# Performance work log

Measured on AMD Instinct MI355X. Metric: run time of the kernel, lower is better.

## Reference

```python
import jax, jax.numpy as jnp
import numpy as np

B, L, D, C, N, K = 4096, 4096, 1024, 64, 8192, 5
TEMP = 0.1
ALPHA = 2.0
EPS = 1e-12


def setup_inputs() -> dict:
    key = jax.random.key(0)
    ks = jax.random.split(key, 8)
    x = jax.random.normal(ks[0], (B, 1, L), jnp.float32)
    y = jax.random.randint(ks[1], (B,), 0, C)
    Wf = jax.random.normal(ks[2], (L, D), jnp.float32) * 0.02
    Wc = jax.random.normal(ks[3], (C, D), jnp.float32) * 0.02
    bc = jnp.zeros((C,), jnp.float32)
    supports_old = jax.random.normal(ks[4], (N, D), jnp.float32)
    scores_old = jax.nn.softmax(jax.random.normal(ks[5], (N, C), jnp.float32), axis=-1)
    labels_old = jax.nn.one_hot(jax.random.randint(ks[6], (N,), 0, C), C, dtype=jnp.float32)
    return dict(x=x, y=y, Wf=Wf, Wc=Wc, bc=bc, supports_old=supports_old,
                labels_old=labels_old, scores_old=scores_old)


def _l2n(v, axis):
    return v / jnp.maximum(jnp.linalg.norm(v, axis=axis, keepdims=True), EPS)


def _masked_mean(v, w):
    return jnp.sum(v * w) / jnp.maximum(jnp.sum(w), 1.0)


def _tta_loss(x, Wf, Wc, bc, supports_old, labels_old, scores_old):
    feats = x.reshape(B, L) @ Wf                      # [B, D] featurizer
    logits = feats @ Wc.T + bc                        # [B, C]
    probs = jax.nn.softmax(logits, -1)
    logp = jax.nn.log_softmax(logits, -1)
    prob = probs.max(-1)
    pred = jnp.argmax(logits, -1)
    # prediction-confidence filter
    y_certain = prob >= prob.mean()
    # input-energy entropy filter (scipy.stats.entropy over axis=2)
    px = x * x
    px = px / jnp.maximum(px.sum(2, keepdims=True), EPS)
    e = -(px * jnp.log(px + 1e-30)).sum(2).reshape(B)
    e_certain = e < e.mean()
    w_c = (e_certain & y_certain).astype(jnp.float32)  # certain mask as weights
    w_u = 1.0 - w_c
    yhat = jax.nn.one_hot(pred, C, dtype=jnp.float32)
    # --- memory bank concat + prototype build (no_grad in torch) ---
    sup_all = jnp.concatenate([supports_old, feats], 0)        # [N+B, D]
    lab_all = jnp.concatenate([labels_old, yhat], 0)           # [N+B, C]
    w_all = jnp.concatenate([jnp.ones((N,), jnp.float32), w_c], 0)
    lw = lab_all * w_all[:, None]
    protos = _l2n(sup_all, 1).T @ lw / jnp.maximum(lw.sum(0, keepdims=True), EPS)
    protos = jax.lax.stop_gradient(_l2n(protos, 0))            # [D, C]
    # --- loss1: Tsallis entropy - diversity on balanced probs ---
    m = jnp.sum(probs * w_c[:, None], 0) / jnp.maximum(w_c.sum(), 1.0)
    pb = probs / jnp.maximum(m, EPS)
    pb = pb / pb.sum(1, keepdims=True)
    tsallis = jnp.mean((1.0 - jnp.sum(pb ** ALPHA, 1)) / (ALPHA - 1.0))
    pm = pb.mean(0)
    div = -jnp.sum(pm * jnp.log(pm + EPS))
    loss1 = tsallis - div
    # --- loss2: PCL, prototype CE on certain samples (temp=1) ---
    lp = jax.nn.log_softmax(_l2n(feats, 1) @ protos, -1)       # [B, C]
    ce = -jnp.take_along_axis(lp, pred[:, None], 1)[:, 0]
    loss2 = _masked_mean(ce, w_c)
    # --- loss3: NCL, kNN soft targets from memory bank, uncertain rows ---
    scores_all = jax.lax.stop_gradient(jnp.concatenate([scores_old, probs], 0))
    sup_det = jax.lax.stop_gradient(sup_all)
    sim = _l2n(feats, 1) @ _l2n(sup_det, 1).T / TEMP           # [B, N+B]
    sim = jnp.where(w_all[None, :] > 0, sim, -jnp.inf)
    _, idx = jax.lax.top_k(sim, K)                             # [B, K]
    tgt = scores_all[idx].mean(1)                              # [B, C]
    ncl = -(tgt * logp).sum(1)
    loss3 = _masked_mean(ncl, w_u)
    return loss1 + loss2 + loss3


def reference(x, y, Wf, Wc, bc, supports_old, labels_old, scores_old):
    return _tta_loss(x, Wf, Wc, bc, supports_old, labels_old, scores_old)
```

## Files before the change

kernel.cpp:

```cpp
#include <hip/hip_runtime.h>
#include <math.h>

#define BBATCH 4096
#define LLEN   4096
#define DDIM   1024
#define CCLS   64
#define NSUP   8192
#define NTOT   12288
#define FEPS   1e-12f
#define KCHUNK 48
#define KCAND  (KCHUNK*6)

#define SC_SUMP  0
#define SC_SUME  1
#define SC_SUMWC 2
#define SC_TSAL  3
#define SC_L2NUM 4
#define SC_L3NUM 5

typedef _Float16 half4_t __attribute__((ext_vector_type(4)));
typedef _Float16 half8_t __attribute__((ext_vector_type(8)));
typedef float    f32x4   __attribute__((ext_vector_type(4)));
typedef float    f32x16  __attribute__((ext_vector_type(16)));

static const size_t OFF_FEATS  = 0;
static const size_t OFF_FEATP1 = OFF_FEATS  + (size_t)BBATCH*DDIM;
static const size_t OFF_WFTH   = OFF_FEATP1 + (size_t)BBATCH*DDIM;
static const size_t OFF_WFTL   = OFF_WFTH   + (size_t)DDIM*LLEN/2;
static const size_t OFF_PROBS  = OFF_WFTL   + (size_t)DDIM*LLEN/2;
static const size_t OFF_LOGP   = OFF_PROBS  + (size_t)BBATCH*CCLS;
static const size_t OFF_FNORM  = OFF_LOGP   + (size_t)BBATCH*CCLS;
static const size_t OFF_SNORM  = OFF_FNORM  + BBATCH;
static const size_t OFF_PMAX   = OFF_SNORM  + NSUP;
static const size_t OFF_EROW   = OFF_PMAX   + BBATCH;
static const size_t OFF_WC     = OFF_EROW   + BBATCH;
static const size_t OFF_PRED   = OFF_WC     + BBATCH;
static const size_t OFF_RB     = OFF_PRED   + BBATCH;
static const size_t OFF_SNM    = OFF_RB     + BBATCH;
static const size_t OFF_PROTOT = OFF_SNM    + NTOT;
static const size_t OFF_CVAL   = OFF_PROTOT + (size_t)CCLS*DDIM;
static const size_t OFF_CIDX   = OFF_CVAL   + (size_t)BBATCH*KCAND;
static const size_t OFF_ZERO   = OFF_CIDX   + (size_t)BBATCH*KCAND;
static const size_t OFF_MACC   = OFF_ZERO;
static const size_t OFF_PMACC  = OFF_MACC   + CCLS;
static const size_t OFF_COLS   = OFF_PMACC  + CCLS;
static const size_t OFF_SCAL   = OFF_COLS   + CCLS;
static const size_t OFF_PROTUN = OFF_SCAL   + 32;
static const size_t OFF_ZEND   = OFF_PROTUN + (size_t)DDIM*CCLS;
static const size_t OFF_SUPH   = OFF_ZEND;
static const size_t OFF_SUPL   = OFF_SUPH   + (size_t)NSUP*DDIM/2;
static const size_t WS_END     = OFF_SUPL   + (size_t)NSUP*DDIM/2;

__device__ __forceinline__ float waveSum(float v){
  #pragma unroll
  for (int o = 32; o > 0; o >>= 1) v += __shfl_xor(v, o);
  return v;
}
__device__ __forceinline__ float waveMax(float v){
  #pragma unroll
  for (int o = 32; o > 0; o >>= 1) v = fmaxf(v, __shfl_xor(v, o));
  return v;
}
__device__ __forceinline__ float blockSum256(float v, float* sh4){
  v = waveSum(v);
  if ((threadIdx.x & 63) == 0) sh4[threadIdx.x >> 6] = v;
  __syncthreads();
  float r = sh4[0] + sh4[1] + sh4[2] + sh4[3];
  __syncthreads();
  return r;
}
__device__ __forceinline__ void top6_insert(float* v, int* ix, float s, int si){
  bool c0=s>v[0],c1=s>v[1],c2=s>v[2],c3=s>v[3],c4=s>v[4],c5=s>v[5];
  v[5]=c5?(c4?v[4]:s):v[5]; ix[5]=c5?(c4?ix[4]:si):ix[5];
  v[4]=c4?(c3?v[3]:s):v[4]; ix[4]=c4?(c3?ix[3]:si):ix[4];
  v[3]=c3?(c2?v[2]:s):v[3]; ix[3]=c3?(c2?ix[2]:si):ix[3];
  v[2]=c2?(c1?v[1]:s):v[2]; ix[2]=c2?(c1?ix[1]:si):ix[2];
  v[1]=c1?(c0?v[0]:s):v[1]; ix[1]=c1?(c0?ix[0]:si):ix[1];
  v[0]=c0?s:v[0];           ix[0]=c0?si:ix[0];
}
__device__ __forceinline__ void split4(const float4 v, half4_t* h, half4_t* l){
  half4_t hh, ll;
  hh[0] = (_Float16)v.x; hh[1] = (_Float16)v.y; hh[2] = (_Float16)v.z; hh[3] = (_Float16)v.w;
  ll[0] = (_Float16)(v.x - (float)hh[0]);
  ll[1] = (_Float16)(v.y - (float)hh[1]);
  ll[2] = (_Float16)(v.z - (float)hh[2]);
  ll[3] = (_Float16)(v.w - (float)hh[3]);
  *h = hh; *l = ll;
}
__device__ __forceinline__ void split8(const float4 a, const float4 b,
                                       half8_t* h, half8_t* l){
  half8_t hh, ll;
  hh[0]=(_Float16)a.x; hh[1]=(_Float16)a.y; hh[2]=(_Float16)a.z; hh[3]=(_Float16)a.w;
  hh[4]=(_Float16)b.x; hh[5]=(_Float16)b.y; hh[6]=(_Float16)b.z; hh[7]=(_Float16)b.w;
  ll[0]=(_Float16)(a.x-(float)hh[0]); ll[1]=(_Float16)(a.y-(float)hh[1]);
  ll[2]=(_Float16)(a.z-(float)hh[2]); ll[3]=(_Float16)(a.w-(float)hh[3]);
  ll[4]=(_Float16)(b.x-(float)hh[4]); ll[5]=(_Float16)(b.y-(float)hh[5]);
  ll[6]=(_Float16)(b.z-(float)hh[6]); ll[7]=(_Float16)(b.w-(float)hh[7]);
  *h = hh; *l = ll;
}

__global__ __launch_bounds__(256)
void k_entropy(const float* __restrict__ x, float* __restrict__ e_row,
               float* __restrict__ scal){
  __shared__ __align__(16) float lx[LLEN];
  __shared__ float sh4[4];
  int row = blockIdx.x, t = threadIdx.x;
  const float4* xr = (const float4*)(x + (size_t)row * LLEN);
  float s = 0.f;
  #pragma unroll
  for (int i = 0; i < 4; ++i){
    float4 v = xr[t + 256*i];
    ((float4*)lx)[t + 256*i] = v;
    s += v.x*v.x + v.y*v.y + v.z*v.z + v.w*v.w;
  }
  s = blockSum256(s, sh4);
  float inv = 1.0f / fmaxf(s, FEPS);
  float ent = 0.f;
  #pragma unroll
  for (int i = 0; i < 4; ++i){
    float4 v = ((float4*)lx)[t + 256*i];
    float p;
    p = v.x*v.x*inv; ent -= p * logf(p + 1e-30f);
    p = v.y*v.y*inv; ent -= p * logf(p + 1e-30f);
    p = v.z*v.z*inv; ent -= p * logf(p + 1e-30f);
    p = v.w*v.w*inv; ent -= p * logf(p + 1e-30f);
  }
  ent = blockSum256(ent, sh4);
  if (t == 0){ e_row[row] = ent; atomicAdd(&scal[SC_SUME], ent); }
}

__global__ __launch_bounds__(256)
void k_wft(const float* __restrict__ Wf, unsigned short* __restrict__ WftH,
           unsigned short* __restrict__ WftL){
  __shared__ __align__(16) float ld[64*68];
  int t = threadIdx.x;
  int d0 = blockIdx.x * 64;
  int l0 = blockIdx.y * 64;
  #pragma unroll
  for (int i = 0; i < 4; ++i){
    int flat = t + 256*i;
    int l = flat >> 4, d4 = (flat & 15) * 4;
    *(float4*)&ld[l*68 + d4] = *(const float4*)(Wf + (size_t)(l0+l)*DDIM + d0 + d4);
  }
  __syncthreads();
  #pragma unroll
  for (int i = 0; i < 4; ++i){
    int flat = t + 256*i;
    int d = flat >> 4, l4 = (flat & 15) * 4;
    float4 v = make_float4(ld[(l4+0)*68 + d], ld[(l4+1)*68 + d],
                           ld[(l4+2)*68 + d], ld[(l4+3)*68 + d]);
    half4_t h, l;
    split4(v, &h, &l);
    *(half4_t*)(WftH + (size_t)(d0+d)*LLEN + l0 + l4) = h;
    *(half4_t*)(WftL + (size_t)(d0+d)*LLEN + l0 + l4) = l;
  }
}

#define SUBH 4096

__global__ __launch_bounds__(256)
void k_feats_mfma(const float* __restrict__ X, const unsigned short* __restrict__ WftHu,
                  const unsigned short* __restrict__ WftLu, float* __restrict__ featp){
  __shared__ __align__(16) _Float16 lds[2*4*SUBH];
  int t = threadIdx.x;
  int n0 = blockIdx.x * 128;
  int m0 = blockIdx.y * 128;
  int kz = blockIdx.z;
  int w = t >> 6, lane = t & 63;
  int wr = w >> 1, wc = w & 1;
  int l31 = lane & 31, hi = lane >> 5;
  const _Float16* Bgh = (const _Float16*)WftHu + (size_t)n0*LLEN;
  const _Float16* Bgl = (const _Float16*)WftLu + (size_t)n0*LLEN;
  const size_t glRow = (size_t)(lane >> 2)*LLEN;
  int ra = t >> 1;
  int kg8 = (t & 1) * 16;
  int aswz = (ra >> 3) & 3;
  const float* Ag = X + (size_t)(m0 + ra)*LLEN + kg8;
  f32x16 acc[2][2];
  #pragma unroll
  for (int i=0;i<2;++i){
    #pragma unroll
    for (int j=0;j<2;++j) acc[i][j] = (f32x16)(0.f);
  }
  const int kstart = kz*2048;

  #define STAGE_B(bufi, k0c) do {                                                 \
    _Float16* Lb = lds + (bufi)*(4*SUBH);                                         \
    _Pragma("unroll")                                                             \
    for (int s2 = 0; s2 < 2; ++s2){                                               \
      int blk = s2*4 + w;                                                         \
      int csrc = (lane & 3) ^ ((blk*2 + (lane >> 5)) & 3);                        \
      size_t go = glRow + (size_t)blk*16*LLEN + (k0c) + (size_t)csrc*8;           \
      __builtin_amdgcn_global_load_lds(                                           \
        (const __attribute__((address_space(1))) void*)(Bgh + go),                \
        (__attribute__((address_space(3))) void*)(Lb + 2*SUBH + blk*512), 16,0,0);\
      __builtin_amdgcn_global_load_lds(                                           \
        (const __attribute__((address_space(1))) void*)(Bgl + go),                \
        (__attribute__((address_space(3))) void*)(Lb + 3*SUBH + blk*512), 16,0,0);\
    }                                                                             \
  } while(0)

  STAGE_B(0, kstart);
  float4 avs[4];
  #pragma unroll
  for (int i=0;i<4;++i) avs[i] = *(const float4*)(Ag + kstart + 4*i);
  int cur = 0;
  int swz = (l31 >> 3) & 3;
  for (int it = 0; it < 64; ++it){
    _Float16* Ah = lds + cur*(4*SUBH);
    _Float16* Al = Ah + SUBH;
    #pragma unroll
    for (int c2 = 0; c2 < 2; ++c2){
      half8_t hv, lv;
      split8(avs[2*c2], avs[2*c2+1], &hv, &lv);
      int slot = ((kg8 >> 3) + c2) ^ aswz;
      *(half8_t*)&Ah[ra*32 + slot*8] = hv;
      *(half8_t*)&Al[ra*32 + slot*8] = lv;
    }
    __syncthreads();
    if (it < 63){
      int kn = kstart + (it+1)*32;
      STAGE_B(cur ^ 1, kn);
      #pragma unroll
      for (int i=0;i<4;++i) avs[i] = *(const float4*)(Ag + kn + 4*i);
      __builtin_amdgcn_sched_barrier(0);
    }
    const _Float16* Bh = lds + cur*(4*SUBH) + 2*SUBH;
    const _Float16* Bl = Bh + SUBH;
    #pragma unroll
    for (int kf = 0; kf < 2; ++kf){
      int sc = (kf*2 + hi) ^ swz;
      half8_t ahf[2], alf[2], bhf[2], blf[2];
      #pragma unroll
      for (int mi=0;mi<2;++mi){
        int off = (wr*64 + mi*32 + l31)*32 + sc*8;
        ahf[mi] = *(const half8_t*)&Ah[off];
        alf[mi] = *(const half8_t*)&Al[off];
      }
      #pragma unroll
      for (int ni=0;ni<2;++ni){
        int off = (wc*64 + ni*32 + l31)*32 + sc*8;
        bhf[ni] = *(const half8_t*)&Bh[off];
        blf[ni] = *(const half8_t*)&Bl[off];
      }
      #pragma unroll
      for (int mi=0;mi<2;++mi){
        #pragma unroll
        for (int ni=0;ni<2;++ni){
          acc[mi][ni] = __builtin_amdgcn_mfma_f32_32x32x16_f16(ahf[mi], bhf[ni], acc[mi][ni], 0,0,0);
          acc[mi][ni] = __builtin_amdgcn_mfma_f32_32x32x16_f16(ahf[mi], blf[ni], acc[mi][ni], 0,0,0);
          acc[mi][ni] = __builtin_amdgcn_mfma_f32_32x32x16_f16(alf[mi], bhf[ni], acc[mi][ni], 0,0,0);
        }
      }
    }
    cur ^= 1;
  }
  #undef STAGE_B
  float* outp = featp + (size_t)kz * BBATCH * DDIM;
  #pragma unroll
  for (int mi=0;mi<2;++mi){
    #pragma unroll
    for (int ni=0;ni<2;++ni){
      #pragma unroll
      for (int r=0;r<16;++r){
        int row = m0 + wr*64 + mi*32 + (r&3) + 8*(r>>2) + 4*hi;
        int col = n0 + wc*64 + ni*32 + l31;
        outp[(size_t)row*DDIM + col] = acc[mi][ni][r];
      }
    }
  }
}

__global__ __launch_bounds__(256)
void k_supnorm(const float* __restrict__ sup, float* __restrict__ snorm,
               _Float16* __restrict__ suph, _Float16* __restrict__ supl){
  int w = threadIdx.x >> 6, lane = threadIdx.x & 63;
  int row = blockIdx.x*4 + w;
  const float4* rp = (const float4*)(sup + (size_t)row * DDIM);
  float s = 0.f;
  #pragma unroll
  for (int j=0;j<4;++j){
    float4 v = rp[lane + 64*j];
    half4_t h, l;
    split4(v, &h, &l);
    *(half4_t*)(suph + (size_t)row*DDIM + (lane + 64*j)*4) = h;
    *(half4_t*)(supl + (size_t)row*DDIM + (lane + 64*j)*4) = l;
    s += v.x*v.x+v.y*v.y+v.z*v.z+v.w*v.w;
  }
  s = waveSum(s);
  if (lane==0) snorm[row] = sqrtf(s);
}

__global__ __launch_bounds__(256)
void k_logits(float* __restrict__ feats, const float* __restrict__ featp1,
              const float* __restrict__ Wc,
              const float* __restrict__ bc, float* __restrict__ probs,
              float* __restrict__ logp, float* __restrict__ pmax,
              int* __restrict__ pred, float* __restrict__ fnorm,
              float* __restrict__ scal,
              _Float16* __restrict__ fh, _Float16* __restrict__ fl){
  __shared__ __align__(16) float f[DDIM];
  __shared__ float z[CCLS];
  __shared__ float sh4[4];
  int row = blockIdx.x, t = threadIdx.x;
  const float4* fr0 = (const float4*)(feats  + (size_t)row * DDIM);
  const float4* fr1 = (const float4*)(featp1 + (size_t)row * DDIM);
  float ss = 0.f;
  { float4 a = fr0[t], b = fr1[t];
    float4 v = make_float4(a.x+b.x, a.y+b.y, a.z+b.z, a.w+b.w);
    ((float4*)f)[t] = v;
    ((float4*)(feats + (size_t)row*DDIM))[t] = v;
    half4_t h, l;
    split4(v, &h, &l);
    *(half4_t*)(fh + (size_t)row*DDIM + t*4) = h;
    *(half4_t*)(fl + (size_t)row*DDIM + t*4) = l;
    ss += v.x*v.x+v.y*v.y+v.z*v.z+v.w*v.w; }
  ss = blockSum256(ss, sh4);
  if (t==0) fnorm[row] = sqrtf(ss);
  int w = t >> 6, lane = t & 63;
  for (int ci = 0; ci < 16; ++ci){
    int c = w*16 + ci;
    const float4* wc = (const float4*)(Wc + (size_t)c * DDIM);
    float d = 0.f;
    #pragma unroll
    for (int j=0;j<4;++j){
      float4 a = wc[lane + 64*j];
      float4 b = ((float4*)f)[lane + 64*j];
      d += a.x*b.x+a.y*b.y+a.z*b.z+a.w*b.w;
    }
    d = waveSum(d);
    if (lane == 0) z[c] = d + bc[c];
  }
  __syncthreads();
  if (w == 0){
    float zz = z[lane];
    float m = waveMax(zz);
    unsigned long long bal = __ballot(zz == m);
    int am = __ffsll(bal) - 1;
    float ex = expf(zz - m);
    float sv = waveSum(ex);
    probs[(size_t)row*CCLS + lane] = ex / sv;
    logp[(size_t)row*CCLS + lane]  = (zz - m) - logf(sv);
    if (lane == 0){
      float pmv = 1.0f / sv;
      pmax[row] = pmv;
      pred[row] = am;
      atomicAdd(&scal[SC_SUMP], pmv);
    }
  }
}

__global__ __launch_bounds__(256)
void k_mask(const float* __restrict__ e_row, const float* __restrict__ pmax,
            const float* __restrict__ fnorm, const float* __restrict__ snorm,
            const int* __restrict__ pred, float* __restrict__ w_c,
            float* __restrict__ rb, float* __restrict__ snm,
            float* __restrict__ colsum, float* __restrict__ scal){
  int i = blockIdx.x * 256 + threadIdx.x;
  if (i < NSUP) snm[i] = 1.0f / fmaxf(snorm[i], FEPS);
  if (i < BBATCH){
    float me = scal[SC_SUME] * (1.0f/BBATCH);
    float mp = scal[SC_SUMP] * (1.0f/BBATCH);
    float wc = ((e_row[i] < me) && (pmax[i] >= mp)) ? 1.0f : 0.0f;
    w_c[i] = wc;
    float fn = fmaxf(fnorm[i], FEPS);
    rb[i] = 10.0f / fn;
    snm[NSUP + i] = (wc > 0.f) ? (1.0f / fn) : -1.0f;
    atomicAdd(&scal[SC_SUMWC], wc);
    atomicAdd(&colsum[pred[i]], wc);
  }
}

__global__ __launch_bounds__(256)
void k_colsum_labels(const float* __restrict__ labels, float* __restrict__ colsum){
  int t = threadIdx.x, c = t & 63, sub = t >> 6;
  int r0 = blockIdx.x * 256;
  float s = 0.f;
  for (int i = 0; i < 64; ++i){
    int r = r0 + sub + 4*i;
    s += labels[(size_t)r*CCLS + c];
  }
  __shared__ float loc[4][64];
  loc[sub][c] = s;
  __syncthreads();
  if (sub == 0) atomicAdd(&colsum[c], loc[0][c]+loc[1][c]+loc[2][c]+loc[3][c]);
}

__global__ __launch_bounds__(256)
void k_m_accum(const float* __restrict__ probs, const float* __restrict__ w_c,
               float* __restrict__ m_acc){
  int t = threadIdx.x, c = t & 63, sub = t >> 6;
  int r0 = blockIdx.x * 64;
  float s = 0.f;
  for (int i = 0; i < 16; ++i){
    int r = r0 + sub + 4*i;
    s += probs[(size_t)r*CCLS + c] * w_c[r];
  }
  __shared__ float loc[4][64];
  loc[sub][c] = s;
  __syncthreads();
  if (sub == 0) atomicAdd(&m_acc[c], loc[0][c]+loc[1][c]+loc[2][c]+loc[3][c]);
}

__global__ __launch_bounds__(256)
void k_loss1(const float* __restrict__ probs, const float* __restrict__ m_acc,
             float* __restrict__ pm_acc, float* __restrict__ scal){
  int t = threadIdx.x, w = t >> 6, lane = t & 63;
  float swc = fmaxf(scal[SC_SUMWC], 1.0f);
  float minv = 1.0f / fmaxf(m_acc[lane] / swc, FEPS);
  float pml = 0.f, tsl = 0.f;
  int r0 = blockIdx.x * 64 + w * 16;
  for (int i = 0; i < 16; ++i){
    int r = r0 + i;
    float pb = probs[(size_t)r*CCLS + lane] * minv;
    float t1 = waveSum(pb);
    float t2 = waveSum(pb*pb);
    tsl += 1.0f - t2/(t1*t1);
    pml += pb/t1;
  }
  atomicAdd(&pm_acc[lane], pml);
  if (lane == 0) atomicAdd(&scal[SC_TSAL], tsl);
}

__global__ __launch_bounds__(256)
void k_protos_gemm(const float* __restrict__ sup, const float* __restrict__ feats,
                   const float* __restrict__ labels, const int* __restrict__ pred,
                   const float* __restrict__ w_c, const float* __restrict__ snm,
                   float* __restrict__ protos_un){
  __shared__ __align__(16) float ssx[64*68];
  __shared__ __align__(16) float sl[64*68];
  int t = threadIdx.x;
  int d0 = blockIdx.x * 64;
  int nbase = blockIdx.y * 1536;
  int dg = t & 15, cg = t >> 4;
  float acc[4][4];
  #pragma unroll
  for (int i=0;i<4;++i){
    #pragma unroll
    for (int j=0;j<4;++j) acc[i][j]=0.f;
  }
  for (int n0 = 0; n0 < 1536; n0 += 64){
    __syncthreads();
    #pragma unroll
    for (int i = 0; i < 4; ++i){
      int fidx = t + 256*i;
      int r = fidx >> 4;
      int dc = (fidx & 15) * 4;
      int n = nbase + n0 + r;
      const float* rp = (n < NSUP) ? (sup + (size_t)n*DDIM)
                                   : (feats + (size_t)(n-NSUP)*DDIM);
      *(float4*)&ssx[r*68 + dc] = *(const float4*)(rp + d0 + dc);
    }
    #pragma unroll
    for (int i = 0; i < 4; ++i){
      int fidx = t + 256*i;
      int r = fidx >> 4;
      int cc = (fidx & 15) * 4;
      int n = nbase + n0 + r;
      float sc = snm[n];
      float4 v;
      if (n < NSUP){
        float4 lb = *(const float4*)(labels + (size_t)n*CCLS + cc);
        v.x = lb.x*sc; v.y = lb.y*sc; v.z = lb.z*sc; v.w = lb.w*sc;
      } else {
        int b = n - NSUP;
        float base = w_c[b] * sc;
        int p = pred[b];
        v.x = (p == cc+0) ? base : 0.f;
        v.y = (p == cc+1) ? base : 0.f;
        v.z = (p == cc+2) ? base : 0.f;
        v.w = (p == cc+3) ? base : 0.f;
      }
      *(float4*)&sl[r*68 + cc] = v;
    }
    __syncthreads();
    #pragma unroll 4
    for (int kk = 0; kk < 64; ++kk){
      float4 a = *(float4*)&ssx[kk*68 + 4*dg];
      float4 b = *(float4*)&sl[kk*68 + 4*cg];
      float av[4] = {a.x,a.y,a.z,a.w};
      float bv[4] = {b.x,b.y,b.z,b.w};
      #pragma unroll
      for (int i=0;i<4;++i){
        #pragma unroll
        for (int j=0;j<4;++j) acc[i][j] = fmaf(av[i], bv[j], acc[i][j]);
      }
    }
  }
  #pragma unroll
  for (int i=0;i<4;++i){
    #pragma unroll
    for (int j=0;j<4;++j)
      atomicAdd(&protos_un[(size_t)(d0 + 4*dg + i)*CCLS + 4*cg + j], acc[i][j]);
  }
}

__global__ __launch_bounds__(256)
void k_protos_norm(const float* __restrict__ protos_un, const float* __restrict__ colsum,
                   float* __restrict__ protos_t){
  int c = blockIdx.x, t = threadIdx.x;
  __shared__ float sh4[4];
  float cs = fmaxf(colsum[c], FEPS);
  float v[4];
  float ss = 0.f;
  #pragma unroll
  for (int i=0;i<4;++i){
    int d = t + 256*i;
    v[i] = protos_un[(size_t)d*CCLS + c] / cs;
    ss += v[i]*v[i];
  }
  ss = blockSum256(ss, sh4);
  float inv = 1.0f / fmaxf(sqrtf(ss), FEPS);
  #pragma unroll
  for (int i=0;i<4;++i){
    int d = t + 256*i;
    protos_t[(size_t)c*DDIM + d] = v[i]*inv;
  }
}

__global__ __launch_bounds__(256)
void k_loss2(const float* __restrict__ feats, const float* __restrict__ protos_t,
             const int* __restrict__ pred, const float* __restrict__ w_c,
             const float* __restrict__ fnorm, float* __restrict__ scal){
  int row = blockIdx.x, t = threadIdx.x;
  float wc = w_c[row];
  if (wc == 0.f) return;
  __shared__ __align__(16) float f[DDIM];
  __shared__ float z[CCLS];
  float inv = 1.0f / fmaxf(fnorm[row], FEPS);
  { float4 v = ((const float4*)(feats + (size_t)row*DDIM))[t];
    v.x*=inv; v.y*=inv; v.z*=inv; v.w*=inv;
    ((float4*)f)[t] = v; }
  __syncthreads();
  int w = t >> 6, lane = t & 63;
  for (int ci=0; ci<16; ++ci){
    int c = w*16+ci;
    const float4* pc = (const float4*)(protos_t + (size_t)c*DDIM);
    float d = 0.f;
    #pragma unroll
    for (int j=0;j<4;++j){
      float4 a = pc[lane + 64*j];
      float4 b = ((float4*)f)[lane + 64*j];
      d += a.x*b.x+a.y*b.y+a.z*b.z+a.w*b.w;
    }
    d = waveSum(d);
    if (lane==0) z[c] = d;
  }
  __syncthreads();
  if (w == 0){
    float zz = z[lane];
    float m = waveMax(zz);
    float sv = waveSum(expf(zz - m));
    if (lane == 0){
      float lse = m + logf(sv);
      float ce = lse - z[pred[row]];
      atomicAdd(&scal[SC_L2NUM], ce * wc);
    }
  }
}

__global__ __launch_bounds__(1024, 1)
void k_sim_approx(const _Float16* __restrict__ fh, const _Float16* __restrict__ suph,
                  const float* __restrict__ snm,
                  float* __restrict__ cval, int* __restrict__ cidx){
  __shared__ __align__(16) _Float16 lds[2*16384];
  __shared__ float sns[256];
  int t = threadIdx.x;
  int w = t >> 6, lane = t & 63;
  int wr = w >> 2, wcn = w & 3;
  int l31 = lane & 31, hi = lane >> 5;
  int bidl = blockIdx.y * 48 + blockIdx.x;
  int xcd = bidl & 7, lin = bidl >> 3;
  int yb = xcd * 2 + (lin / 48);
  int xb = lin - (lin / 48) * 48;
  int m0 = xb * 256, n0 = yb * 256;
  if (t < 256) sns[t] = snm[m0 + t];
  const _Float16* Ag = (xb < 32) ? (suph + (size_t)m0*DDIM)
                                 : (fh + (size_t)(m0-NSUP)*DDIM);
  const _Float16* Bg = fh + (size_t)n0*DDIM;
  int Rs = w*16 + (lane>>2);
  int cs = (lane & 3) ^ ((Rs >> 3) & 3);
  const size_t offS = (size_t)Rs*DDIM + (size_t)cs*8;
  f32x16 acc[2][2];
  #pragma unroll
  for (int i=0;i<2;++i){
    #pragma unroll
    for (int j=0;j<2;++j) acc[i][j] = (f32x16)(0.f);
  }

  #define SIM_ST(b, kt) do {                                                      \
    __builtin_amdgcn_global_load_lds(                                             \
      (const __attribute__((address_space(1))) void*)(Ag + offS + (size_t)(kt)*32),\
      (__attribute__((address_space(3))) void*)(lds + (b)*16384 + w*512), 16,0,0);\
    __builtin_amdgcn_global_load_lds(                                             \
      (const __attribute__((address_space(1))) void*)(Bg + offS + (size_t)(kt)*32),\
      (__attribute__((address_space(3))) void*)(lds + (b)*16384 + 8192 + w*512), 16,0,0);\
  } while(0)

  SIM_ST(0, 0);
  for (int kt = 0; kt < 32; ++kt){
    const _Float16* buf = lds + (kt&1)*16384;
    __syncthreads();
    half8_t af[2][2], bf[2][2];
    #pragma unroll
    for (int p=0;p<2;++p){
      int Ra = wr*64 + p*32 + l31;
      int sw = (Ra>>3)&3;
      #pragma unroll
      for (int kf=0;kf<2;++kf)
        af[p][kf] = *(const half8_t*)(buf + Ra*32 + (((kf*2+hi)^sw))*8);
    }
    #pragma unroll
    for (int ni=0;ni<2;++ni){
      int Rb = wcn*64 + ni*32 + l31;
      int sw = (Rb>>3)&3;
      #pragma unroll
      for (int kf=0;kf<2;++kf)
        bf[ni][kf] = *(const half8_t*)(buf + 8192 + Rb*32 + (((kf*2+hi)^sw))*8);
    }
    if (kt < 31) SIM_ST((kt+1)&1, kt+1);
    __builtin_amdgcn_s_setprio(1);
    #pragma unroll
    for (int p=0;p<2;++p){
      #pragma unroll
      for (int ni=0;ni<2;++ni){
        #pragma unroll
        for (int kf=0;kf<2;++kf)
          acc[p][ni] = __builtin_amdgcn_mfma_f32_32x32x16_f16(af[p][kf], bf[ni][kf], acc[p][ni], 0,0,0);
      }
    }
    __builtin_amdgcn_s_setprio(0);
  }
  #undef SIM_ST
  __syncthreads();
  float tv[2][6]; int ti[2][6];
  #pragma unroll
  for (int ni=0;ni<2;++ni){
    #pragma unroll
    for (int k=0;k<6;++k){ tv[ni][k] = -INFINITY; ti[ni][k] = 0x7fffffff; }
  }
  #pragma unroll
  for (int ni=0;ni<2;++ni){
    #pragma unroll
    for (int p=0;p<2;++p){
      #pragma unroll
      for (int r=0;r<16;++r){
        int rl = wr*64 + p*32 + (r&3) + 8*(r>>2) + 4*hi;
        float sn = sns[rl];
        float v = acc[p][ni][r] * fabsf(sn);
        v = (sn > 0.f) ? v : -INFINITY;
        top6_insert(tv[ni], ti[ni], v, m0 + rl);
      }
    }
  }
  #pragma unroll
  for (int ni=0;ni<2;++ni){
    float pv[6]; int pi[6];
    #pragma unroll
    for (int k=0;k<6;++k){ pv[k] = __shfl_xor(tv[ni][k], 32); pi[k] = __shfl_xor(ti[ni][k], 32); }
    #pragma unroll
    for (int k=0;k<6;++k) top6_insert(tv[ni], ti[ni], pv[k], pi[k]);
  }
  float* MV = (float*)lds;
  int*   MI = (int*)((char*)lds + 24576);
  if (hi == 0){
    #pragma unroll
    for (int ni=0;ni<2;++ni){
      int col = wcn*64 + ni*32 + l31;
      #pragma unroll
      for (int k=0;k<6;++k){
        MV[(col*4 + wr)*6 + k] = tv[ni][k];
        MI[(col*4 + wr)*6 + k] = ti[ni][k];
      }
    }
  }
  __syncthreads();
  if (t < 256){
    float bv[6]; int bi[6];
    #pragma unroll
    for (int k=0;k<6;++k){ bv[k] = -INFINITY; bi[k] = 0x7fffffff; }
    for (int j = 0; j < 24; ++j) top6_insert(bv, bi, MV[t*24 + j], MI[t*24 + j]);
    float* co = cval + (size_t)(n0 + t)*KCAND + xb*6;
    int*   ci = cidx + (size_t)(n0 + t)*KCAND + xb*6;
    #pragma unroll
    for (int k=0;k<6;++k){ co[k] = bv[k]; ci[k] = bi[k]; }
  }
}

__global__ __launch_bounds__(256)
void k_rescore_ncl(const float* __restrict__ cval, const int* __restrict__ cidx,
                   const float* __restrict__ sup, const float* __restrict__ feats,
                   const float* __restrict__ rb, const float* __restrict__ snm,
                   const float* __restrict__ scores_old, const float* __restrict__ probs,
                   const float* __restrict__ logp, const float* __restrict__ w_c,
                   float* __restrict__ scal){
  int t = threadIdx.x, w = t >> 6, lane = t & 63;
  int b = blockIdx.x*4 + w;
  float lv[5]; int li[5];
  #pragma unroll
  for (int j=0;j<5;++j){
    int idx = lane + 64*j;
    bool ok = idx < KCAND;
    lv[j] = ok ? cval[(size_t)b*KCAND + idx] : -INFINITY;
    li[j] = ok ? cidx[(size_t)b*KCAND + idx] : 0x7fffffff;
  }
  #pragma unroll
  for (int a=0;a<4;++a){
    #pragma unroll
    for (int c=0;c<4-a;++c){
      bool sw = lv[c+1] > lv[c];
      float fv = sw ? lv[c+1] : lv[c];  float fw = sw ? lv[c] : lv[c+1];
      int   iv = sw ? li[c+1] : li[c];  int   iw = sw ? li[c] : li[c+1];
      lv[c]=fv; lv[c+1]=fw; li[c]=iv; li[c+1]=iw;
    }
  }
  float t10v[10]; int t10i[10];
  int head = 0;
  #pragma unroll
  for (int k=0;k<10;++k){
    float hv = -INFINITY; int hidx = 0x7fffffff;
    switch(head){
      case 0: hv=lv[0]; hidx=li[0]; break;
      case 1: hv=lv[1]; hidx=li[1]; break;
      case 2: hv=lv[2]; hidx=li[2]; break;
      case 3: hv=lv[3]; hidx=li[3]; break;
      case 4: hv=lv[4]; hidx=li[4]; break;
      default: break;
    }
    float m = waveMax(hv);
    unsigned long long bal = __ballot(hv == m);
    int wl = __ffsll(bal) - 1;
    t10v[k] = m;
    t10i[k] = __shfl(hidx, wl);
    if (lane == wl) head++;
  }
  (void)t10v;
  float4 fr0 = *(const float4*)(feats + (size_t)b*DDIM + lane*16);
  float4 fr1 = *(const float4*)(feats + (size_t)b*DDIM + lane*16 + 4);
  float4 fr2 = *(const float4*)(feats + (size_t)b*DDIM + lane*16 + 8);
  float4 fr3 = *(const float4*)(feats + (size_t)b*DDIM + lane*16 + 12);
  float rbv = rb[b];
  float ev[10];
  #pragma unroll
  for (int c=0;c<10;++c){
    int idx = t10i[c];
    const float* srow = (idx < NSUP) ? (sup + (size_t)idx*DDIM)
                                     : (feats + (size_t)(idx-NSUP)*DDIM);
    float4 s0 = *(const float4*)(srow + lane*16);
    float4 s1 = *(const float4*)(srow + lane*16 + 4);
    float4 s2 = *(const float4*)(srow + lane*16 + 8);
    float4 s3 = *(const float4*)(srow + lane*16 + 12);
    float d = fr0.x*s0.x + fr0.y*s0.y + fr0.z*s0.z + fr0.w*s0.w
            + fr1.x*s1.x + fr1.y*s1.y + fr1.z*s1.z + fr1.w*s1.w
            + fr2.x*s2.x + fr2.y*s2.y + fr2.z*s2.z + fr2.w*s2.w
            + fr3.x*s3.x + fr3.y*s3.y + fr3.z*s3.z + fr3.w*s3.w;
    d = waveSum(d);
    ev[c] = d * rbv * fabsf(snm[idx]);
  }
  int used = 0;
  int sel[5];
  #pragma unroll
  for (int k=0;k<5;++k){
    float bb = -INFINITY; int bbi = 0x7fffffff; int bj = 0;
    #pragma unroll
    for (int j=0;j<10;++j){
      bool free_ = !((used >> j) & 1);
      bool better = free_ && ((ev[j] > bb) || (ev[j] == bb && t10i[j] < bbi));
      bb  = better ? ev[j]   : bb;
      bbi = better ? t10i[j] : bbi;
      bj  = better ? j       : bj;
    }
    used |= (1 << bj);
    sel[k] = bbi;
  }
  float tg = 0.f;
  #pragma unroll
  for (int k=0;k<5;++k){
    int ix = sel[k];
    const float* srow = (ix < NSUP) ? (scores_old + (size_t)ix*CCLS)
                                    : (probs + (size_t)(ix-NSUP)*CCLS);
    tg += srow[lane];
  }
  tg *= 0.2f;
  float d = tg * logp[(size_t)b*CCLS + lane];
  d = waveSum(d);
  if (lane == 0) atomicAdd(&scal[SC_L3NUM], -d * (1.0f - w_c[b]));
}

__global__ void k_final(const float* __restrict__ pm_acc, const float* __restrict__ scal,
                        float* __restrict__ out){
  int lane = threadIdx.x;
  float pm = pm_acc[lane] * (1.0f/BBATCH);
  float dterm = pm * logf(pm + FEPS);
  float dv = waveSum(dterm);
  if (lane == 0){
    float div = -dv;
    float tsallis = scal[SC_TSAL] * (1.0f/BBATCH);
    float swc = scal[SC_SUMWC];
    float l1 = tsallis - div;
    float l2 = scal[SC_L2NUM] / fmaxf(swc, 1.0f);
    float l3 = scal[SC_L3NUM] / fmaxf((float)BBATCH - swc, 1.0f);
    out[0] = l1 + l2 + l3;
  }
}

extern "C" void kernel_launch(void* const* d_in, const int* in_sizes, int n_in,
                              void* d_out, int out_size, void* d_ws, size_t ws_size,
                              hipStream_t stream){
  (void)in_sizes; (void)n_in; (void)out_size; (void)ws_size;
  const float* x      = (const float*)d_in[0];
  const float* Wf     = (const float*)d_in[2];
  const float* Wc     = (const float*)d_in[3];
  const float* bc     = (const float*)d_in[4];
  const float* sup    = (const float*)d_in[5];
  const float* labels = (const float*)d_in[6];
  const float* scores = (const float*)d_in[7];
  float* ws = (float*)d_ws;

  float* feats  = ws + OFF_FEATS;
  float* featp1 = ws + OFF_FEATP1;
  unsigned short* wfth = (unsigned short*)(ws + OFF_WFTH);
  unsigned short* wftl = (unsigned short*)(ws + OFF_WFTL);
  _Float16* feat_h = (_Float16*)(ws + OFF_WFTH);
  _Float16* feat_l = (_Float16*)(ws + OFF_WFTL);
  _Float16* sup_h  = (_Float16*)(ws + OFF_SUPH);
  _Float16* sup_l  = (_Float16*)(ws + OFF_SUPL);
  float* probs  = ws + OFF_PROBS;
  float* logp   = ws + OFF_LOGP;
  float* fnorm  = ws + OFF_FNORM;
  float* snorm  = ws + OFF_SNORM;
  float* pmax   = ws + OFF_PMAX;
  float* e_row  = ws + OFF_EROW;
  float* w_c    = ws + OFF_WC;
  int*   pred   = (int*)(ws + OFF_PRED);
  float* rb     = ws + OFF_RB;
  float* snm    = ws + OFF_SNM;
  float* protot = ws + OFF_PROTOT;
  float* cvalp  = ws + OFF_CVAL;
  int*   cidxp  = (int*)(ws + OFF_CIDX);
  float* m_acc  = ws + OFF_MACC;
  float* pm_acc = ws + OFF_PMACC;
  float* colsum = ws + OFF_COLS;
  float* scal   = ws + OFF_SCAL;
  float* protun = ws + OFF_PROTUN;

  hipMemsetAsync(ws + OFF_ZERO, 0, (OFF_ZEND - OFF_ZERO)*sizeof(float), stream);

  k_entropy      <<<BBATCH, 256, 0, stream>>>(x, e_row, scal);
  k_wft          <<<dim3(DDIM/64, LLEN/64), 256, 0, stream>>>(Wf, wfth, wftl);
  k_feats_mfma   <<<dim3(DDIM/128, BBATCH/128, 2), 256, 0, stream>>>(x, wfth, wftl, feats);
  k_supnorm      <<<NSUP/4, 256, 0, stream>>>(sup, snorm, sup_h, sup_l);
  k_logits       <<<BBATCH, 256, 0, stream>>>(feats, featp1, Wc, bc, probs, logp, pmax, pred, fnorm, scal, feat_h, feat_l);
  k_mask         <<<32, 256, 0, stream>>>(e_row, pmax, fnorm, snorm, pred, w_c, rb, snm, colsum, scal);
  k_colsum_labels<<<32, 256, 0, stream>>>(labels, colsum);
  k_m_accum      <<<64, 256, 0, stream>>>(probs, w_c, m_acc);
  k_loss1        <<<64, 256, 0, stream>>>(probs, m_acc, pm_acc, scal);
  k_protos_gemm  <<<dim3(16, 8), 256, 0, stream>>>(sup, feats, labels, pred, w_c, snm, protun);
  k_protos_norm  <<<CCLS, 256, 0, stream>>>(protun, colsum, protot);
  k_loss2        <<<BBATCH, 256, 0, stream>>>(feats, protot, pred, w_c, fnorm, scal);
  k_sim_approx   <<<dim3(48, 16), 1024, 0, stream>>>(feat_h, sup_h, snm, cvalp, cidxp);
  k_rescore_ncl  <<<BBATCH/4, 256, 0, stream>>>(cvalp, cidxp, sup, feats, rb, snm, scores, probs, logp, w_c, scal);
  k_final        <<<1, 64, 0, stream>>>(pm_acc, scal, (float*)d_out);
}
```

Baseline: 826.7 us.

## Store fp16 sims operands in k-tiled swizzled layout, drop unused low halves

Support and feature fp16 copies are now written into one buffer laid out by 32-wide k-tiles with an XOR swizzle, so each k-step of the similarity GEMM loads a contiguous block per wave instead of strided rows. The unused low-half fp16 residual writes for supports and features are removed, which cuts write traffic in k_supnorm and k_logits. The LDS merge buffers for top-6 candidates are padded to a 25 stride to reduce bank conflicts. Producers now do scattered 8-byte writes into the tiled layout, which may coalesce less well.

```diff
diff --git a/kernel.cpp b/kernel.cpp
--- a/kernel.cpp
+++ b/kernel.cpp
@@ -47,9 +47,8 @@
 static const size_t OFF_SCAL   = OFF_COLS   + CCLS;
 static const size_t OFF_PROTUN = OFF_SCAL   + 32;
 static const size_t OFF_ZEND   = OFF_PROTUN + (size_t)DDIM*CCLS;
-static const size_t OFF_SUPH   = OFF_ZEND;
-static const size_t OFF_SUPL   = OFF_SUPH   + (size_t)NSUP*DDIM/2;
-static const size_t WS_END     = OFF_SUPL   + (size_t)NSUP*DDIM/2;
+static const size_t OFF_HT     = OFF_ZEND;
+static const size_t WS_END     = OFF_HT + (size_t)32*NTOT*32/2;
 
 __device__ __forceinline__ float waveSum(float v){
   #pragma unroll
@@ -97,6 +96,11 @@
   ll[4]=(_Float16)(b.x-(float)hh[4]); ll[5]=(_Float16)(b.y-(float)hh[5]);
   ll[6]=(_Float16)(b.z-(float)hh[6]); ll[7]=(_Float16)(b.w-(float)hh[7]);
   *h = hh; *l = ll;
+}
+__device__ __forceinline__ size_t ht_off(int row, int d){
+  int kt = d >> 5;
+  int slot = ((d >> 3) & 3) ^ ((row >> 3) & 3);
+  return (size_t)kt * (NTOT*32) + (size_t)row * 32 + slot*8 + (d & 7);
 }
 
 __global__ __launch_bounds__(256)
@@ -273,7 +277,7 @@
 
 __global__ __launch_bounds__(256)
 void k_supnorm(const float* __restrict__ sup, float* __restrict__ snorm,
-               _Float16* __restrict__ suph, _Float16* __restrict__ supl){
+               _Float16* __restrict__ ht){
   int w = threadIdx.x >> 6, lane = threadIdx.x & 63;
   int row = blockIdx.x*4 + w;
   const float4* rp = (const float4*)(sup + (size_t)row * DDIM);
@@ -281,10 +285,10 @@
   #pragma unroll
   for (int j=0;j<4;++j){
     float4 v = rp[lane + 64*j];
-    half4_t h, l;
-    split4(v, &h, &l);
-    *(half4_t*)(suph + (size_t)row*DDIM + (lane + 64*j)*4) = h;
-    *(half4_t*)(supl + (size_t)row*DDIM + (lane + 64*j)*4) = l;
+    half4_t h;
+    h[0]=(_Float16)v.x; h[1]=(_Float16)v.y; h[2]=(_Float16)v.z; h[3]=(_Float16)v.w;
+    int d = (lane + 64*j)*4;
+    *(half4_t*)(ht + ht_off(row, d)) = h;
     s += v.x*v.x+v.y*v.y+v.z*v.z+v.w*v.w;
   }
   s = waveSum(s);
@@ -298,7 +302,7 @@
               float* __restrict__ logp, float* __restrict__ pmax,
               int* __restrict__ pred, float* __restrict__ fnorm,
               float* __restrict__ scal,
-              _Float16* __restrict__ fh, _Float16* __restrict__ fl){
+              _Float16* __restrict__ ht){
   __shared__ __align__(16) float f[DDIM];
   __shared__ float z[CCLS];
   __shared__ float sh4[4];
@@ -310,10 +314,9 @@
     float4 v = make_float4(a.x+b.x, a.y+b.y, a.z+b.z, a.w+b.w);
     ((float4*)f)[t] = v;
     ((float4*)(feats + (size_t)row*DDIM))[t] = v;
-    half4_t h, l;
-    split4(v, &h, &l);
-    *(half4_t*)(fh + (size_t)row*DDIM + t*4) = h;
-    *(half4_t*)(fl + (size_t)row*DDIM + t*4) = l;
+    half4_t h;
+    h[0]=(_Float16)v.x; h[1]=(_Float16)v.y; h[2]=(_Float16)v.z; h[3]=(_Float16)v.w;
+    *(half4_t*)(ht + ht_off(NSUP + row, t*4)) = h;
     ss += v.x*v.x+v.y*v.y+v.z*v.z+v.w*v.w; }
   ss = blockSum256(ss, sh4);
   if (t==0) fnorm[row] = sqrtf(ss);
@@ -560,8 +563,7 @@
 }
 
 __global__ __launch_bounds__(1024, 1)
-void k_sim_approx(const _Float16* __restrict__ fh, const _Float16* __restrict__ suph,
-                  const float* __restrict__ snm,
+void k_sim_approx(const _Float16* __restrict__ ht, const float* __restrict__ snm,
                   float* __restrict__ cval, int* __restrict__ cidx){
   __shared__ __align__(16) _Float16 lds[2*16384];
   __shared__ float sns[256];
@@ -575,12 +577,8 @@
   int xb = lin - (lin / 48) * 48;
   int m0 = xb * 256, n0 = yb * 256;
   if (t < 256) sns[t] = snm[m0 + t];
-  const _Float16* Ag = (xb < 32) ? (suph + (size_t)m0*DDIM)
-                                 : (fh + (size_t)(m0-NSUP)*DDIM);
-  const _Float16* Bg = fh + (size_t)n0*DDIM;
-  int Rs = w*16 + (lane>>2);
-  int cs = (lane & 3) ^ ((Rs >> 3) & 3);
-  const size_t offS = (size_t)Rs*DDIM + (size_t)cs*8;
+  const _Float16* Abase = ht + (size_t)(m0 + w*16)*32 + (size_t)lane*8;
+  const _Float16* Bbase = ht + (size_t)(NSUP + n0 + w*16)*32 + (size_t)lane*8;
   f32x16 acc[2][2];
   #pragma unroll
   for (int i=0;i<2;++i){
@@ -590,10 +588,10 @@
 
   #define SIM_ST(b, kt) do {                                                      \
     __builtin_amdgcn_global_load_lds(                                             \
-      (const __attribute__((address_space(1))) void*)(Ag + offS + (size_t)(kt)*32),\
+      (const __attribute__((address_space(1))) void*)(Abase + (size_t)(kt)*(NTOT*32)),\
       (__attribute__((address_space(3))) void*)(lds + (b)*16384 + w*512), 16,0,0);\
     __builtin_amdgcn_global_load_lds(                                             \
-      (const __attribute__((address_space(1))) void*)(Bg + offS + (size_t)(kt)*32),\
+      (const __attribute__((address_space(1))) void*)(Bbase + (size_t)(kt)*(NTOT*32)),\
       (__attribute__((address_space(3))) void*)(lds + (b)*16384 + 8192 + w*512), 16,0,0);\
   } while(0)
 
@@ -662,15 +660,15 @@
     for (int k=0;k<6;++k) top6_insert(tv[ni], ti[ni], pv[k], pi[k]);
   }
   float* MV = (float*)lds;
-  int*   MI = (int*)((char*)lds + 24576);
+  int*   MI = (int*)lds + 6400;
   if (hi == 0){
     #pragma unroll
     for (int ni=0;ni<2;++ni){
       int col = wcn*64 + ni*32 + l31;
       #pragma unroll
       for (int k=0;k<6;++k){
-        MV[(col*4 + wr)*6 + k] = tv[ni][k];
-        MI[(col*4 + wr)*6 + k] = ti[ni][k];
+        MV[col*25 + wr*6 + k] = tv[ni][k];
+        MI[col*25 + wr*6 + k] = ti[ni][k];
       }
     }
   }
@@ -679,7 +677,7 @@
     float bv[6]; int bi[6];
     #pragma unroll
     for (int k=0;k<6;++k){ bv[k] = -INFINITY; bi[k] = 0x7fffffff; }
-    for (int j = 0; j < 24; ++j) top6_insert(bv, bi, MV[t*24 + j], MI[t*24 + j]);
+    for (int j = 0; j < 24; ++j) top6_insert(bv, bi, MV[t*25 + j], MI[t*25 + j]);
     float* co = cval + (size_t)(n0 + t)*KCAND + xb*6;
     int*   ci = cidx + (size_t)(n0 + t)*KCAND + xb*6;
     #pragma unroll
@@ -821,10 +819,7 @@
   float* featp1 = ws + OFF_FEATP1;
   unsigned short* wfth = (unsigned short*)(ws + OFF_WFTH);
   unsigned short* wftl = (unsigned short*)(ws + OFF_WFTL);
-  _Float16* feat_h = (_Float16*)(ws + OFF_WFTH);
-  _Float16* feat_l = (_Float16*)(ws + OFF_WFTL);
-  _Float16* sup_h  = (_Float16*)(ws + OFF_SUPH);
-  _Float16* sup_l  = (_Float16*)(ws + OFF_SUPL);
+  _Float16* ht  = (_Float16*)(ws + OFF_HT);
   float* probs  = ws + OFF_PROBS;
   float* logp   = ws + OFF_LOGP;
   float* fnorm  = ws + OFF_FNORM;
@@ -849,8 +844,8 @@
   k_entropy      <<<BBATCH, 256, 0, stream>>>(x, e_row, scal);
   k_wft          <<<dim3(DDIM/64, LLEN/64), 256, 0, stream>>>(Wf, wfth, wftl);
   k_feats_mfma   <<<dim3(DDIM/128, BBATCH/128, 2), 256, 0, stream>>>(x, wfth, wftl, feats);
-  k_supnorm      <<<NSUP/4, 256, 0, stream>>>(sup, snorm, sup_h, sup_l);
-  k_logits       <<<BBATCH, 256, 0, stream>>>(feats, featp1, Wc, bc, probs, logp, pmax, pred, fnorm, scal, feat_h, feat_l);
+  k_supnorm      <<<NSUP/4, 256, 0, stream>>>(sup, snorm, ht);
+  k_logits       <<<BBATCH, 256, 0, stream>>>(feats, featp1, Wc, bc, probs, logp, pmax, pred, fnorm, scal, ht);
   k_mask         <<<32, 256, 0, stream>>>(e_row, pmax, fnorm, snorm, pred, w_c, rb, snm, colsum, scal);
   k_colsum_labels<<<32, 256, 0, stream>>>(labels, colsum);
   k_m_accum      <<<64, 256, 0, stream>>>(probs, w_c, m_acc);
@@ -858,7 +853,7 @@
   k_protos_gemm  <<<dim3(16, 8), 256, 0, stream>>>(sup, feats, labels, pred, w_c, snm, protun);
   k_protos_norm  <<<CCLS, 256, 0, stream>>>(protun, colsum, protot);
   k_loss2        <<<BBATCH, 256, 0, stream>>>(feats, protot, pred, w_c, fnorm, scal);
-  k_sim_approx   <<<dim3(48, 16), 1024, 0, stream>>>(feat_h, sup_h, snm, cvalp, cidxp);
+  k_sim_approx   <<<dim3(48, 16), 1024, 0, stream>>>(ht, snm, cvalp, cidxp);
   k_rescore_ncl  <<<BBATCH/4, 256, 0, stream>>>(cvalp, cidxp, sup, feats, rb, snm, scores, probs, logp, w_c, scal);
   k_final        <<<1, 64, 0, stream>>>(pm_acc, scal, (float*)d_out);
 }
```

Result: no change. 819.7 us (-0.8%).
